# Kernel optimization log

Measured on AMD Instinct MI355X. Metric: run time of the kernel, lower is better.

Reference implementation:

```python
import jax, jax.numpy as jnp
import numpy as np

B, L, D, H = 2, 2048, 1024, 16
DK = D // H  # head_dim = 64


def setup_inputs() -> dict:
    key = jax.random.key(0)
    ks = jax.random.split(key, 12)
    init = lambda k, shape, fan_in: jax.random.uniform(k, shape, jnp.float32, -1.0, 1.0) / np.sqrt(fan_in)
    inp = {
        "query": jax.random.normal(ks[0], (B, L, D), jnp.float32),
        "key": jax.random.normal(ks[1], (B, L, D), jnp.float32),
        "value": jax.random.normal(ks[2], (B, L, D), jnp.float32),
        # causal mask [B, 1, L, L], True = attend
        "mask": jnp.broadcast_to(jnp.tril(jnp.ones((L, L), bool))[None, None], (B, 1, L, L)),
        "wq": init(ks[3], (D, D), D), "bq": jnp.zeros((D,), jnp.float32),
        "wk": init(ks[4], (D, D), D), "bk": jnp.zeros((D,), jnp.float32),
        "wv": init(ks[5], (D, D), D), "bv": jnp.zeros((D,), jnp.float32),
        "wo": init(ks[6], (D, D), D), "bo": jnp.zeros((D,), jnp.float32),
    }
    return inp


def reference(query, key, value, mask, wq, bq, wk, bk, wv, bv, wo, bo):
    b, l, d = query.shape
    split = lambda x: x.reshape(b, l, H, DK).transpose(0, 2, 1, 3)  # B H L dk
    Q = split(query @ wq + bq)
    K = split(key @ wk + bk)
    V = split(value @ wv + bv)
    scores = jnp.einsum("bhqd,bhkd->bhqk", Q, K) / jnp.sqrt(jnp.float32(DK))
    probs = jax.nn.softmax(scores, axis=-1, where=mask)  # masked-out rows contribute 0
    attn = jnp.einsum("bhqk,bhkd->bhqd", probs, V)
    out = attn.transpose(0, 2, 1, 3).reshape(b, l, d)  # B L D
    return out @ wo + bo
```

## Files before the change

### kernel.cpp

```cpp
#include <hip/hip_runtime.h>
#include <hip/hip_bf16.h>

typedef __bf16 bf16x8 __attribute__((ext_vector_type(8)));
typedef __bf16 bf16x4 __attribute__((ext_vector_type(4)));
typedef float floatx4 __attribute__((ext_vector_type(4)));

constexpr int Bn  = 2;
constexpr int Ln  = 2048;
constexpr int Dn  = 1024;
constexpr int Hn  = 16;
constexpr int DKn = 64;
constexpr int Mn  = Bn * Ln;

__device__ __forceinline__ void gload_lds16(const void* g, void* l) {
  __builtin_amdgcn_global_load_lds(
      (const __attribute__((address_space(1))) void*)g,
      (__attribute__((address_space(3))) void*)l, 16, 0, 0);
}

__global__ __launch_bounds__(256) void prep_w(
    const float* __restrict__ wq, const float* __restrict__ wk,
    const float* __restrict__ wv, const float* __restrict__ wo,
    __hip_bfloat16* __restrict__ wT)
{
  const int z = blockIdx.z;
  const float* src = z == 0 ? wq : z == 1 ? wk : z == 2 ? wv : wo;
  __hip_bfloat16* dst = wT + (size_t)z * Dn * Dn;
  __shared__ __bf16 tile[32][33];
  const int bx = blockIdx.x & 31, by = blockIdx.x >> 5;
  const int tx = threadIdx.x & 31, ty = threadIdx.x >> 5;
  const int x = bx * 32 + tx, y = by * 32 + ty;
  for (int i = 0; i < 32; i += 8)
    tile[ty + i][tx] = (__bf16)src[(size_t)(y + i) * Dn + x];
  __syncthreads();
  const int x2 = by * 32 + tx, y2 = bx * 32 + ty;
  for (int i = 0; i < 32; i += 8)
    ((__bf16*)dst)[(size_t)(y2 + i) * Dn + x2] = tile[tx][ty + i];
}

__global__ __launch_bounds__(256) void gemm_qkv(
    const float* __restrict__ q, const float* __restrict__ k,
    const float* __restrict__ v,
    const __hip_bfloat16* __restrict__ wT,
    const float* __restrict__ bq, const float* __restrict__ bk,
    const float* __restrict__ bv,
    __hip_bfloat16* __restrict__ Qp, __hip_bfloat16* __restrict__ Kp,
    __hip_bfloat16* __restrict__ Vt)
{
  constexpr int BK = 32, LDA = 40;
  __shared__ __align__(16) __bf16 As[128][LDA];
  __shared__ __bf16 Ws[128][BK];
  const int z = blockIdx.z;
  const float* A = z == 0 ? q : z == 1 ? k : v;
  const __hip_bfloat16* WT = wT + (size_t)z * Dn * Dn;
  const float* bias = z == 0 ? bq : z == 1 ? bk : bv;

  const int m0 = blockIdx.x * 128;
  const int n0 = blockIdx.y * 128;
  const int tid  = threadIdx.x;
  const int lane = tid & 63;
  const int wave = tid >> 6;
  const int quad = lane >> 4;
  const int l16  = lane & 15;
  const int wm = (wave >> 1) * 64;
  const int wn = (wave & 1) * 64;
  const int srow = tid >> 2;
  const int scol = (tid & 3) * 8;
  const int arow = tid >> 1;
  const int akh  = (tid & 1) * 16;

  floatx4 acc[4][4];
  for (int i = 0; i < 4; i++)
    for (int j = 0; j < 4; j++)
      acc[i][j] = (floatx4){0.f, 0.f, 0.f, 0.f};

  for (int k0 = 0; k0 < Dn; k0 += BK) {
    for (int half = 0; half < 2; half++)
      gload_lds16(&WT[(size_t)(n0 + srow + half * 64) * Dn + k0 + scol],
                  &Ws[srow + half * 64][scol]);
    const float* ap = &A[(size_t)(m0 + arow) * Dn + k0 + akh];
    const float4 f0 = *(const float4*)(ap + 0);
    const float4 f1 = *(const float4*)(ap + 4);
    const float4 f2 = *(const float4*)(ap + 8);
    const float4 f3 = *(const float4*)(ap + 12);
    bf16x8 v0, v1;
    v0[0] = (__bf16)f0.x; v0[1] = (__bf16)f0.y; v0[2] = (__bf16)f0.z; v0[3] = (__bf16)f0.w;
    v0[4] = (__bf16)f1.x; v0[5] = (__bf16)f1.y; v0[6] = (__bf16)f1.z; v0[7] = (__bf16)f1.w;
    v1[0] = (__bf16)f2.x; v1[1] = (__bf16)f2.y; v1[2] = (__bf16)f2.z; v1[3] = (__bf16)f2.w;
    v1[4] = (__bf16)f3.x; v1[5] = (__bf16)f3.y; v1[6] = (__bf16)f3.z; v1[7] = (__bf16)f3.w;
    *(bf16x8*)&As[arow][akh]     = v0;
    *(bf16x8*)&As[arow][akh + 8] = v1;
    __syncthreads();
    bf16x8 af[4], wf[4];
    for (int i = 0; i < 4; i++) af[i] = *(const bf16x8*)&As[wm + i * 16 + l16][quad * 8];
    for (int j = 0; j < 4; j++) wf[j] = *(const bf16x8*)&Ws[wn + j * 16 + l16][quad * 8];
    if (z == 2) {
      for (int i = 0; i < 4; i++)
        for (int j = 0; j < 4; j++)
          acc[i][j] = __builtin_amdgcn_mfma_f32_16x16x32_bf16(af[i], wf[j], acc[i][j], 0, 0, 0);
    } else {
      for (int i = 0; i < 4; i++)
        for (int j = 0; j < 4; j++)
          acc[i][j] = __builtin_amdgcn_mfma_f32_16x16x32_bf16(wf[j], af[i], acc[i][j], 0, 0, 0);
    }
    __syncthreads();
  }

  if (z == 2) {
    for (int j = 0; j < 4; j++) {
      const int n = n0 + wn + j * 16 + l16;
      const float bvv = bias[n];
      const int h = n >> 6, dk = n & 63;
      for (int i = 0; i < 4; i++) {
        const int m = m0 + wm + i * 16 + quad * 4;
        const int b = m >> 11, li = m & (Ln - 1);
        bf16x4 pk;
        for (int r = 0; r < 4; r++) pk[r] = (__bf16)(acc[i][j][r] + bvv);
        *(bf16x4*)&Vt[(((size_t)(b * Hn + h)) * DKn + dk) * Ln + li] = pk;
      }
    }
  } else {
    __hip_bfloat16* out = z == 0 ? Qp : Kp;
    for (int j = 0; j < 4; j++) {
      const int nq = n0 + wn + j * 16 + quad * 4;
      const float4 b4 = *(const float4*)&bias[nq];
      const int h = nq >> 6, dk = nq & 63;
      for (int i = 0; i < 4; i++) {
        const int m = m0 + wm + i * 16 + l16;
        const int b = m >> 11, li = m & (Ln - 1);
        bf16x4 pk;
        pk[0] = (__bf16)(acc[i][j][0] + b4.x);
        pk[1] = (__bf16)(acc[i][j][1] + b4.y);
        pk[2] = (__bf16)(acc[i][j][2] + b4.z);
        pk[3] = (__bf16)(acc[i][j][3] + b4.w);
        *(bf16x4*)&out[(((size_t)(b * Hn + h)) * Ln + li) * DKn + dk] = pk;
      }
    }
  }
}

__global__ __launch_bounds__(256) void gemm_out(
    const __hip_bfloat16* __restrict__ A,
    const __hip_bfloat16* __restrict__ WT,
    const float* __restrict__ bias,
    float* __restrict__ out)
{
  constexpr int BK = 32;
  __shared__ __bf16 As[128][BK];
  __shared__ __bf16 Ws[64][BK];
  const int m0 = blockIdx.x * 128;
  const int n0 = blockIdx.y * 64;
  const int tid  = threadIdx.x;
  const int lane = tid & 63;
  const int wave = tid >> 6;
  const int quad = lane >> 4;
  const int l16  = lane & 15;
  const int wm = (wave >> 1) * 64;
  const int wn = (wave & 1) * 32;
  const int srow = tid >> 2;
  const int scol = (tid & 3) * 8;

  floatx4 acc[4][2];
  for (int i = 0; i < 4; i++)
    for (int j = 0; j < 2; j++)
      acc[i][j] = (floatx4){0.f, 0.f, 0.f, 0.f};

  for (int k0 = 0; k0 < Dn; k0 += BK) {
    for (int half = 0; half < 2; half++)
      gload_lds16(&A [(size_t)(m0 + srow + half * 64) * Dn + k0 + scol],
                  &As[srow + half * 64][scol]);
    gload_lds16(&WT[(size_t)(n0 + srow) * Dn + k0 + scol], &Ws[srow][scol]);
    __syncthreads();
    bf16x8 af[4], wf[2];
    for (int i = 0; i < 4; i++) af[i] = *(const bf16x8*)&As[wm + i * 16 + l16][quad * 8];
    for (int j = 0; j < 2; j++) wf[j] = *(const bf16x8*)&Ws[wn + j * 16 + l16][quad * 8];
    for (int i = 0; i < 4; i++)
      for (int j = 0; j < 2; j++)
        acc[i][j] = __builtin_amdgcn_mfma_f32_16x16x32_bf16(af[i], wf[j], acc[i][j], 0, 0, 0);
    __syncthreads();
  }

  for (int j = 0; j < 2; j++) {
    const int n = n0 + wn + j * 16 + l16;
    const float bvv = bias[n];
    for (int i = 0; i < 4; i++)
      for (int r = 0; r < 4; r++) {
        const int m = m0 + wm + i * 16 + quad * 4 + r;
        out[(size_t)m * Dn + n] = acc[i][j][r] + bvv;
      }
  }
}

__global__ __launch_bounds__(64) void attn_flash(
    const __hip_bfloat16* __restrict__ Qp,
    const __hip_bfloat16* __restrict__ Kp,
    const __hip_bfloat16* __restrict__ Vt,
    __hip_bfloat16* __restrict__ attn)
{
  const int bh   = blockIdx.x;
  const int qt   = gridDim.y - 1 - blockIdx.y;
  const int lane = threadIdx.x & 63;
  const int quad = lane >> 4;
  const int l16  = lane & 15;
  const int qw   = qt * 32;

  const __hip_bfloat16* Qh = Qp + (size_t)bh * Ln * DKn;
  const __hip_bfloat16* Kh = Kp + (size_t)bh * Ln * DKn;
  const __hip_bfloat16* Vh = Vt + (size_t)bh * DKn * Ln;

  __shared__ __align__(16) __bf16 Ks[64][64];
  __shared__ __align__(16) __bf16 Vs[64][64];
  __shared__ __align__(16) __bf16 Plds[2][16][72];

  const int srow8 = lane >> 3;
  const int gch   = (lane & 7) ^ srow8;
  const int xs    = l16 & 7;
  const int b = bh >> 4, h = bh & 15;

  auto stage = [&](int kt) {
    for (int u = 0; u < 8; u++) {
      gload_lds16(Kh + (size_t)(kt + u * 8 + srow8) * DKn + gch * 8,
                  &Ks[u * 8][0] + (size_t)lane * 8);
      gload_lds16(Vh + (size_t)(u * 8 + srow8) * Ln + kt + gch * 8,
                  &Vs[u * 8][0] + (size_t)lane * 8);
    }
  };

  bf16x8 qf[2][2];
  for (int m = 0; m < 2; m++)
    for (int dd = 0; dd < 2; dd++)
      qf[m][dd] = *(const bf16x8*)&Qh[(size_t)(qw + m * 16 + l16) * DKn + dd * 32 + quad * 8];

  floatx4 o[2][4];
  for (int m = 0; m < 2; m++)
    for (int t = 0; t < 4; t++) o[m][t] = (floatx4){0.f, 0.f, 0.f, 0.f};
  float lp[2] = {0.f, 0.f};

  stage(0);
  const int iters = (qt >> 1) + 1;
  for (int it = 0; it < iters; it++) {
    const int kt = it * 64;
    __syncthreads();

    bf16x8 kf[4][2], vf[4][2];
    for (int sub = 0; sub < 4; sub++)
      for (int dd = 0; dd < 2; dd++)
        kf[sub][dd] = *(const bf16x8*)&Ks[sub * 16 + l16][((dd * 4 + quad) ^ xs) * 8];
    for (int t = 0; t < 4; t++)
      for (int kc = 0; kc < 2; kc++)
        vf[t][kc] = *(const bf16x8*)&Vs[t * 16 + l16][((kc * 4 + quad) ^ xs) * 8];

    __syncthreads();
    if (it + 1 < iters) stage(kt + 64);

    floatx4 s[2][4];
    for (int m = 0; m < 2; m++)
      for (int sub = 0; sub < 4; sub++) s[m][sub] = (floatx4){0.f, 0.f, 0.f, 0.f};
    for (int sub = 0; sub < 4; sub++)
      for (int dd = 0; dd < 2; dd++) {
        s[0][sub] = __builtin_amdgcn_mfma_f32_16x16x32_bf16(kf[sub][dd], qf[0][dd], s[0][sub], 0, 0, 0);
        s[1][sub] = __builtin_amdgcn_mfma_f32_16x16x32_bf16(kf[sub][dd], qf[1][dd], s[1][sub], 0, 0, 0);
      }

    for (int m = 0; m < 2; m++) {
      const bool needmask = (kt + 64 > qw + m * 16);
      const int qg = qw + m * 16 + l16;
      for (int sub = 0; sub < 4; sub++) {
        bf16x4 pk;
        for (int r = 0; r < 4; r++) {
          float sv = s[m][sub][r];
          if (needmask && (kt + sub * 16 + quad * 4 + r > qg)) sv = -1e30f;
          const float e = __builtin_exp2f(__builtin_fmaf(sv, 0.18033688f, -11.5415603f));
          lp[m] += e;
          pk[r] = (__bf16)e;
        }
        *(bf16x4*)&Plds[m][l16][sub * 16 + quad * 4] = pk;
      }
    }
    __asm__ volatile("s_waitcnt lgkmcnt(0)" ::: "memory");

    bf16x8 pf[2][2];
    for (int m = 0; m < 2; m++)
      for (int kc = 0; kc < 2; kc++)
        pf[m][kc] = *(const bf16x8*)&Plds[m][l16][kc * 32 + quad * 8];
    for (int m = 0; m < 2; m++)
      for (int t = 0; t < 4; t++)
        for (int kc = 0; kc < 2; kc++)
          o[m][t] = __builtin_amdgcn_mfma_f32_16x16x32_bf16(vf[t][kc], pf[m][kc], o[m][t], 0, 0, 0);
  }

  for (int m = 0; m < 2; m++) {
    float lf = lp[m];
    lf += __shfl_xor(lf, 16);
    lf += __shfl_xor(lf, 32);
    const float inv = 1.0f / lf;
    const int ql = qw + m * 16 + l16;
    const size_t base = ((size_t)b * Ln + ql) * Dn + h * DKn;
    for (int t = 0; t < 4; t++) {
      bf16x4 pk;
      for (int r = 0; r < 4; r++) pk[r] = (__bf16)(o[m][t][r] * inv);
      *(bf16x4*)&attn[base + t * 16 + quad * 4] = pk;
    }
  }
}

extern "C" void kernel_launch(void* const* d_in, const int* in_sizes, int n_in,
                              void* d_out, int out_size, void* d_ws, size_t ws_size,
                              hipStream_t stream) {
  const float* query = (const float*)d_in[0];
  const float* key_  = (const float*)d_in[1];
  const float* value = (const float*)d_in[2];
  const float* wq = (const float*)d_in[4];
  const float* bq = (const float*)d_in[5];
  const float* wk = (const float*)d_in[6];
  const float* bk = (const float*)d_in[7];
  const float* wv = (const float*)d_in[8];
  const float* bv = (const float*)d_in[9];
  const float* wo = (const float*)d_in[10];
  const float* bo = (const float*)d_in[11];

  const size_t T   = (size_t)Mn * Dn;
  const size_t WSZ = (size_t)Dn * Dn;
  __hip_bfloat16* Qp   = (__hip_bfloat16*)d_ws;
  __hip_bfloat16* Kp   = Qp + T;
  __hip_bfloat16* Vt   = Kp + T;
  __hip_bfloat16* attn = Vt + T;
  __hip_bfloat16* wT   = attn + T;

  prep_w<<<dim3(1024, 1, 4), 256, 0, stream>>>(wq, wk, wv, wo, wT);
  gemm_qkv<<<dim3(Mn / 128, Dn / 128, 3), 256, 0, stream>>>(
      query, key_, value, wT, bq, bk, bv, Qp, Kp, Vt);
  attn_flash<<<dim3(Bn * Hn, Ln / 32), 64, 0, stream>>>(Qp, Kp, Vt, attn);
  gemm_out<<<dim3(Mn / 128, Dn / 64), 256, 0, stream>>>(attn, wT + 3 * WSZ, bo, (float*)d_out);
}
```

Measured before the change: 299.1 us.

## Double-buffer QKV GEMM loads and use 4-wave blocks for flash attention

The QKV projection GEMM now prefetches the next A tile into registers and the next W tile into a second LDS buffer while the current tile is computed, which removes one barrier per k-step and hides global load latency. The attention kernel goes from one wave handling 32 query rows to four waves each handling 16 rows of a 64-row tile. The four waves share one K/V stage in LDS and split the staging work. This cuts per-row K/V traffic and raises occupancy, at the cost of intra-block barriers across waves. The diagonal tile is now 64 wide, so the reversed tile ordering that balanced causal work was dropped, which may worsen tail imbalance.

```diff
diff --git a/kernel.cpp b/kernel.cpp
--- a/kernel.cpp
+++ b/kernel.cpp
@@ -49,7 +49,7 @@
 {
   constexpr int BK = 32, LDA = 40;
   __shared__ __align__(16) __bf16 As[128][LDA];
-  __shared__ __bf16 Ws[128][BK];
+  __shared__ __bf16 Ws[2][128][BK];
   const int z = blockIdx.z;
   const float* A = z == 0 ? q : z == 1 ? k : v;
   const __hip_bfloat16* WT = wT + (size_t)z * Dn * Dn;
@@ -74,15 +74,19 @@
     for (int j = 0; j < 4; j++)
       acc[i][j] = (floatx4){0.f, 0.f, 0.f, 0.f};
 
+  const float* aBase = &A[(size_t)(m0 + arow) * Dn + akh];
+  float4 f0 = *(const float4*)(aBase + 0);
+  float4 f1 = *(const float4*)(aBase + 4);
+  float4 f2 = *(const float4*)(aBase + 8);
+  float4 f3 = *(const float4*)(aBase + 12);
+  for (int half = 0; half < 2; half++)
+    gload_lds16(&WT[(size_t)(n0 + srow + half * 64) * Dn + scol],
+                &Ws[0][srow + half * 64][scol]);
+
   for (int k0 = 0; k0 < Dn; k0 += BK) {
-    for (int half = 0; half < 2; half++)
-      gload_lds16(&WT[(size_t)(n0 + srow + half * 64) * Dn + k0 + scol],
-                  &Ws[srow + half * 64][scol]);
-    const float* ap = &A[(size_t)(m0 + arow) * Dn + k0 + akh];
-    const float4 f0 = *(const float4*)(ap + 0);
-    const float4 f1 = *(const float4*)(ap + 4);
-    const float4 f2 = *(const float4*)(ap + 8);
-    const float4 f3 = *(const float4*)(ap + 12);
+    const int wb = (k0 >> 5) & 1;
+    __syncthreads();
+
     bf16x8 v0, v1;
     v0[0] = (__bf16)f0.x; v0[1] = (__bf16)f0.y; v0[2] = (__bf16)f0.z; v0[3] = (__bf16)f0.w;
     v0[4] = (__bf16)f1.x; v0[5] = (__bf16)f1.y; v0[6] = (__bf16)f1.z; v0[7] = (__bf16)f1.w;
@@ -91,9 +95,21 @@
     *(bf16x8*)&As[arow][akh]     = v0;
     *(bf16x8*)&As[arow][akh + 8] = v1;
     __syncthreads();
+
+    if (k0 + BK < Dn) {
+      const float* ap = aBase + k0 + BK;
+      f0 = *(const float4*)(ap + 0);
+      f1 = *(const float4*)(ap + 4);
+      f2 = *(const float4*)(ap + 8);
+      f3 = *(const float4*)(ap + 12);
+      for (int half = 0; half < 2; half++)
+        gload_lds16(&WT[(size_t)(n0 + srow + half * 64) * Dn + k0 + BK + scol],
+                    &Ws[wb ^ 1][srow + half * 64][scol]);
+    }
+
     bf16x8 af[4], wf[4];
     for (int i = 0; i < 4; i++) af[i] = *(const bf16x8*)&As[wm + i * 16 + l16][quad * 8];
-    for (int j = 0; j < 4; j++) wf[j] = *(const bf16x8*)&Ws[wn + j * 16 + l16][quad * 8];
+    for (int j = 0; j < 4; j++) wf[j] = *(const bf16x8*)&Ws[wb][wn + j * 16 + l16][quad * 8];
     if (z == 2) {
       for (int i = 0; i < 4; i++)
         for (int j = 0; j < 4; j++)
@@ -103,7 +119,6 @@
         for (int j = 0; j < 4; j++)
           acc[i][j] = __builtin_amdgcn_mfma_f32_16x16x32_bf16(wf[j], af[i], acc[i][j], 0, 0, 0);
     }
-    __syncthreads();
   }
 
   if (z == 2) {
@@ -191,18 +206,20 @@
   }
 }
 
-__global__ __launch_bounds__(64) void attn_flash(
+__global__ __launch_bounds__(256) void attn_flash(
     const __hip_bfloat16* __restrict__ Qp,
     const __hip_bfloat16* __restrict__ Kp,
     const __hip_bfloat16* __restrict__ Vt,
     __hip_bfloat16* __restrict__ attn)
 {
   const int bh   = blockIdx.x;
-  const int qt   = gridDim.y - 1 - blockIdx.y;
-  const int lane = threadIdx.x & 63;
+  const int qt   = blockIdx.y;
+  const int tid  = threadIdx.x;
+  const int wave = tid >> 6;
+  const int lane = tid & 63;
   const int quad = lane >> 4;
   const int l16  = lane & 15;
-  const int qw   = qt * 32;
+  const int qw   = qt * 64 + wave * 16;
 
   const __hip_bfloat16* Qh = Qp + (size_t)bh * Ln * DKn;
   const __hip_bfloat16* Kh = Kp + (size_t)bh * Ln * DKn;
@@ -210,7 +227,7 @@
 
   __shared__ __align__(16) __bf16 Ks[64][64];
   __shared__ __align__(16) __bf16 Vs[64][64];
-  __shared__ __align__(16) __bf16 Plds[2][16][72];
+  __shared__ __align__(16) __bf16 Plds[4][16][72];
 
   const int srow8 = lane >> 3;
   const int gch   = (lane & 7) ^ srow8;
@@ -218,7 +235,8 @@
   const int b = bh >> 4, h = bh & 15;
 
   auto stage = [&](int kt) {
-    for (int u = 0; u < 8; u++) {
+    for (int s = 0; s < 2; s++) {
+      const int u = wave * 2 + s;
       gload_lds16(Kh + (size_t)(kt + u * 8 + srow8) * DKn + gch * 8,
                   &Ks[u * 8][0] + (size_t)lane * 8);
       gload_lds16(Vh + (size_t)(u * 8 + srow8) * Ln + kt + gch * 8,
@@ -226,18 +244,16 @@
     }
   };
 
-  bf16x8 qf[2][2];
-  for (int m = 0; m < 2; m++)
-    for (int dd = 0; dd < 2; dd++)
-      qf[m][dd] = *(const bf16x8*)&Qh[(size_t)(qw + m * 16 + l16) * DKn + dd * 32 + quad * 8];
-
-  floatx4 o[2][4];
-  for (int m = 0; m < 2; m++)
-    for (int t = 0; t < 4; t++) o[m][t] = (floatx4){0.f, 0.f, 0.f, 0.f};
-  float lp[2] = {0.f, 0.f};
+  bf16x8 qf[2];
+  for (int dd = 0; dd < 2; dd++)
+    qf[dd] = *(const bf16x8*)&Qh[(size_t)(qw + l16) * DKn + dd * 32 + quad * 8];
+
+  floatx4 o[4];
+  for (int t = 0; t < 4; t++) o[t] = (floatx4){0.f, 0.f, 0.f, 0.f};
+  float lp = 0.f;
 
   stage(0);
-  const int iters = (qt >> 1) + 1;
+  const int iters = qt + 1;
   for (int it = 0; it < iters; it++) {
     const int kt = it * 64;
     __syncthreads();
@@ -253,54 +269,45 @@
     __syncthreads();
     if (it + 1 < iters) stage(kt + 64);
 
-    floatx4 s[2][4];
-    for (int m = 0; m < 2; m++)
-      for (int sub = 0; sub < 4; sub++) s[m][sub] = (floatx4){0.f, 0.f, 0.f, 0.f};
+    floatx4 s[4];
+    for (int sub = 0; sub < 4; sub++) s[sub] = (floatx4){0.f, 0.f, 0.f, 0.f};
     for (int sub = 0; sub < 4; sub++)
-      for (int dd = 0; dd < 2; dd++) {
-        s[0][sub] = __builtin_amdgcn_mfma_f32_16x16x32_bf16(kf[sub][dd], qf[0][dd], s[0][sub], 0, 0, 0);
-        s[1][sub] = __builtin_amdgcn_mfma_f32_16x16x32_bf16(kf[sub][dd], qf[1][dd], s[1][sub], 0, 0, 0);
+      for (int dd = 0; dd < 2; dd++)
+        s[sub] = __builtin_amdgcn_mfma_f32_16x16x32_bf16(kf[sub][dd], qf[dd], s[sub], 0, 0, 0);
+
+    const bool needmask = (kt + 64 > qw);
+    const int qg = qw + l16;
+    for (int sub = 0; sub < 4; sub++) {
+      bf16x4 pk;
+      for (int r = 0; r < 4; r++) {
+        float sv = s[sub][r];
+        if (needmask && (kt + sub * 16 + quad * 4 + r > qg)) sv = -1e30f;
+        const float e = __builtin_exp2f(__builtin_fmaf(sv, 0.18033688f, -11.5415603f));
+        lp += e;
+        pk[r] = (__bf16)e;
       }
-
-    for (int m = 0; m < 2; m++) {
-      const bool needmask = (kt + 64 > qw + m * 16);
-      const int qg = qw + m * 16 + l16;
-      for (int sub = 0; sub < 4; sub++) {
-        bf16x4 pk;
-        for (int r = 0; r < 4; r++) {
-          float sv = s[m][sub][r];
-          if (needmask && (kt + sub * 16 + quad * 4 + r > qg)) sv = -1e30f;
-          const float e = __builtin_exp2f(__builtin_fmaf(sv, 0.18033688f, -11.5415603f));
-          lp[m] += e;
-          pk[r] = (__bf16)e;
-        }
-        *(bf16x4*)&Plds[m][l16][sub * 16 + quad * 4] = pk;
-      }
+      *(bf16x4*)&Plds[wave][l16][sub * 16 + quad * 4] = pk;
     }
     __asm__ volatile("s_waitcnt lgkmcnt(0)" ::: "memory");
 
-    bf16x8 pf[2][2];
-    for (int m = 0; m < 2; m++)
+    bf16x8 pf[2];
+    for (int kc = 0; kc < 2; kc++)
+      pf[kc] = *(const bf16x8*)&Plds[wave][l16][kc * 32 + quad * 8];
+    for (int t = 0; t < 4; t++)
       for (int kc = 0; kc < 2; kc++)
-        pf[m][kc] = *(const bf16x8*)&Plds[m][l16][kc * 32 + quad * 8];
-    for (int m = 0; m < 2; m++)
-      for (int t = 0; t < 4; t++)
-        for (int kc = 0; kc < 2; kc++)
-          o[m][t] = __builtin_amdgcn_mfma_f32_16x16x32_bf16(vf[t][kc], pf[m][kc], o[m][t], 0, 0, 0);
-  }
-
-  for (int m = 0; m < 2; m++) {
-    float lf = lp[m];
-    lf += __shfl_xor(lf, 16);
-    lf += __shfl_xor(lf, 32);
-    const float inv = 1.0f / lf;
-    const int ql = qw + m * 16 + l16;
-    const size_t base = ((size_t)b * Ln + ql) * Dn + h * DKn;
-    for (int t = 0; t < 4; t++) {
-      bf16x4 pk;
-      for (int r = 0; r < 4; r++) pk[r] = (__bf16)(o[m][t][r] * inv);
-      *(bf16x4*)&attn[base + t * 16 + quad * 4] = pk;
-    }
+        o[t] = __builtin_amdgcn_mfma_f32_16x16x32_bf16(vf[t][kc], pf[kc], o[t], 0, 0, 0);
+  }
+
+  float lf = lp;
+  lf += __shfl_xor(lf, 16);
+  lf += __shfl_xor(lf, 32);
+  const float inv = 1.0f / lf;
+  const int ql = qw + l16;
+  const size_t base = ((size_t)b * Ln + ql) * Dn + h * DKn;
+  for (int t = 0; t < 4; t++) {
+    bf16x4 pk;
+    for (int r = 0; r < 4; r++) pk[r] = (__bf16)(o[t][r] * inv);
+    *(bf16x4*)&attn[base + t * 16 + quad * 4] = pk;
   }
 }
 
@@ -330,6 +337,6 @@
   prep_w<<<dim3(1024, 1, 4), 256, 0, stream>>>(wq, wk, wv, wo, wT);
   gemm_qkv<<<dim3(Mn / 128, Dn / 128, 3), 256, 0, stream>>>(
       query, key_, value, wT, bq, bk, bv, Qp, Kp, Vt);
-  attn_flash<<<dim3(Bn * Hn, Ln / 32), 64, 0, stream>>>(Qp, Kp, Vt, attn);
+  attn_flash<<<dim3(Bn * Hn, Ln / 64), 256, 0, stream>>>(Qp, Kp, Vt, attn);
   gemm_out<<<dim3(Mn / 128, Dn / 64), 256, 0, stream>>>(attn, wT + 3 * WSZ, bo, (float*)d_out);
 }
```

Result: faster. 291.3 us (-2.6%).
